# Kernel tuning notes

Hardware: AMD Instinct MI355X
Metric: run time of the kernel (lower is better)

The kernel has to match this reference:

```python
import jax, jax.numpy as jnp
import numpy as np

STRIDE, PAD, DIL, KH, KW = 1, 1, 1, 3, 3


def _bilinear_gather(img, y, xq):
    # img: (Cin,H,W); y,xq: (K,Ho,Wo) float sample coords. Zero padding outside.
    H, W = img.shape[1], img.shape[2]
    y0 = jnp.floor(y); x0 = jnp.floor(xq)
    wy1 = y - y0; wx1 = xq - x0
    wy0 = 1.0 - wy1; wx0 = 1.0 - wx1

    def g(yi, xi):
        valid = (yi >= 0) & (yi <= H - 1) & (xi >= 0) & (xi <= W - 1)
        yc = jnp.clip(yi, 0, H - 1).astype(jnp.int32)
        xc = jnp.clip(xi, 0, W - 1).astype(jnp.int32)
        v = img[:, yc, xc]  # (Cin,K,Ho,Wo)
        return jnp.where(valid[None], v, 0.0)

    return ((wy0 * wx0)[None] * g(y0, x0) + (wy0 * wx1)[None] * g(y0, x0 + 1)
            + (wy1 * wx0)[None] * g(y0 + 1, x0) + (wy1 * wx1)[None] * g(y0 + 1, x0 + 1))


def _deform_conv2d(x, offset, weight, bias):
    B, Cin, H, W = x.shape
    Cout = weight.shape[0]
    Ho, Wo = offset.shape[2], offset.shape[3]
    K = KH * KW
    off = offset.reshape(B, K, 2, Ho, Wo)  # (y,x) pairs per kernel tap, row-major
    ki, kj = jnp.meshgrid(jnp.arange(KH), jnp.arange(KW), indexing='ij')
    base_y = (jnp.arange(Ho) * STRIDE - PAD)[None, :, None] + (ki.reshape(K) * DIL)[:, None, None]  # (K,Ho,1)
    base_x = (jnp.arange(Wo) * STRIDE - PAD)[None, None, :] + (kj.reshape(K) * DIL)[:, None, None]  # (K,1,Wo)
    ys = base_y.astype(x.dtype) + off[:, :, 0]  # (B,K,Ho,Wo)
    xs = base_x.astype(x.dtype) + off[:, :, 1]
    samples = jax.vmap(_bilinear_gather)(x, ys, xs)  # (B,Cin,K,Ho,Wo)
    out = jnp.einsum('bckhw,ock->bohw', samples, weight.reshape(Cout, Cin, K))
    return out + bias[None, :, None, None]


def setup_inputs() -> dict:
    key = jax.random.key(0)
    k1, k2, k3, k4, k5 = jax.random.split(key, 5)
    x = jax.random.normal(k1, (8, 64, 96, 96), dtype=jnp.float32)
    offset = jax.random.normal(k2, (8, 18, 96, 96), dtype=jnp.float32)
    x2 = jax.random.normal(k3, (8, 64, 96, 96), dtype=jnp.float32)
    weight = jax.random.normal(k4, (64, 64, 3, 3), dtype=jnp.float32) * 0.04  # ~kaiming scale for fan_in=576
    bias = jax.random.normal(k5, (64,), dtype=jnp.float32) * 0.1
    return {'x': x, 'offset': offset, 'x2': x2, 'weight': weight, 'bias': bias}


def reference(x, offset, x2, weight, bias):
    out = _deform_conv2d(x, offset, weight, bias)
    out = out + x2
    return jnp.clip(out, 0.0, 6.0)  # ReLU6
```

## Files before the change

### kernel.cpp

```cpp
#include <hip/hip_runtime.h>
#include <math.h>

#define B_    8
#define CIN   64
#define COUT  64
#define H_    96
#define W_    96
#define HW    9216
#define KK    9
#define PIX   64
#define NTHR  256
#define BLKS_PER_B 144
#define SP    72

typedef __attribute__((ext_vector_type(8))) short short8;
typedef __attribute__((ext_vector_type(4))) float floatx4;

static __device__ __forceinline__ unsigned short f2bf(float f) {
    unsigned u = __float_as_uint(f);
    unsigned r = (u + 0x7FFFu + ((u >> 16) & 1u)) >> 16;
    return (unsigned short)r;
}
static __device__ __forceinline__ float bf_lo(unsigned u) { return __uint_as_float(u << 16); }
static __device__ __forceinline__ float bf_hi(unsigned u) { return __uint_as_float(u & 0xFFFF0000u); }

__global__ __launch_bounds__(256) void prep_w_kernel(const float* __restrict__ w,
                                                     unsigned short* __restrict__ wA) {
    int gid  = blockIdx.x * 256 + threadIdx.x;
    int lane = gid & 63;
    int wq   = (gid >> 6) & 3;
    int kap  = gid >> 8;
    int o    = wq * 16 + (lane & 15);
    int cb   = (kap & 1) * 32 + (lane >> 4) * 8;
    int tap  = kap >> 1;
    short8 v;
    #pragma unroll
    for (int j = 0; j < 8; ++j)
        v[j] = (short)f2bf(w[o * 576 + (cb + j) * 9 + tap]);
    *(short8*)&wA[(size_t)gid * 8] = v;
}

__global__ __launch_bounds__(256) void nhwc_bf16_kernel(const float* __restrict__ x,
                                                        unsigned int* __restrict__ xTu) {
    __shared__ float tile[64][65];
    int b   = blockIdx.x / BLKS_PER_B;
    int hw0 = (blockIdx.x % BLKS_PER_B) * 64;
    int lane = threadIdx.x & 63;
    int r    = threadIdx.x >> 6;
    const float* xb = x + (size_t)b * CIN * HW;
    #pragma unroll
    for (int i = 0; i < 16; ++i) {
        int c = r + i * 4;
        tile[c][lane] = xb[(size_t)c * HW + hw0 + lane];
    }
    __syncthreads();
    unsigned int* dst = xTu + ((size_t)b * HW + hw0) * 32;
    int c2 = threadIdx.x & 31;
    int pr = threadIdx.x >> 5;
    #pragma unroll
    for (int i = 0; i < 8; ++i) {
        int p = pr + i * 8;
        unsigned pk = (unsigned)f2bf(tile[2 * c2][p]) |
                      ((unsigned)f2bf(tile[2 * c2 + 1][p]) << 16);
        dst[(size_t)p * 32 + c2] = pk;
    }
}

__global__ __launch_bounds__(256, 4) void deform_mfma_kernel(
    const unsigned int* __restrict__ xTu, const float* __restrict__ offset,
    const float* __restrict__ x2, const float* __restrict__ bias,
    const unsigned short* __restrict__ wA, float* __restrict__ out)
{
    __shared__ float4 ew4[KK * PIX];
    __shared__ int4   eo4[KK * PIX];
    __shared__ __align__(16) short S[2][PIX * SP];

    const int tid  = threadIdx.x;
    const int b    = blockIdx.x & 7;
    const int pix0 = (blockIdx.x >> 3) * PIX;
    const int lane = tid & 63;
    const int wq   = __builtin_amdgcn_readfirstlane(tid >> 6);

    const unsigned int* xb = xTu + (size_t)b * HW * 32;
    const float* offb = offset + (size_t)b * (18 * HW);

    const short8* wAv = (const short8*)wA;
    const int abase = wq * 64 + lane;

    short8 a0 = wAv[abase];
    short8 a1 = wAv[abase + 4 * 64];

    for (int e = tid; e < KK * PIX; e += NTHR) {
        int k  = e >> 6;
        int p  = e & 63;
        int hw = pix0 + p;
        int h  = hw / W_;
        int w  = hw - h * W_;
        float offy = offb[(size_t)(2 * k) * HW + hw];
        float offx = offb[(size_t)(2 * k + 1) * HW + hw];
        int ki = k / 3;
        int kj = k - ki * 3;
        float yy = (float)(h - 1 + ki) + offy;
        float xx = (float)(w - 1 + kj) + offx;
        float y0f = floorf(yy), x0f = floorf(xx);
        float wy1 = yy - y0f, wx1 = xx - x0f;
        float wy0 = 1.0f - wy1, wx0 = 1.0f - wx1;
        int y0 = (int)y0f, x0 = (int)x0f;
        int y1 = y0 + 1, x1 = x0 + 1;
        float vy0 = (y0 >= 0 && y0 < H_) ? 1.0f : 0.0f;
        float vy1 = (y1 >= 0 && y1 < H_) ? 1.0f : 0.0f;
        float vx0 = (x0 >= 0 && x0 < W_) ? 1.0f : 0.0f;
        float vx1 = (x1 >= 0 && x1 < W_) ? 1.0f : 0.0f;
        int y0c = min(max(y0, 0), H_ - 1), y1c = min(max(y1, 0), H_ - 1);
        int x0c = min(max(x0, 0), W_ - 1), x1c = min(max(x1, 0), W_ - 1);
        ew4[e] = make_float4(wy0 * wx0 * vy0 * vx0,
                             wy0 * wx1 * vy0 * vx1,
                             wy1 * wx0 * vy1 * vx0,
                             wy1 * wx1 * vy1 * vx1);
        eo4[e] = make_int4(y0c * W_ + x0c, y0c * W_ + x1c,
                           y1c * W_ + x0c, y1c * W_ + x1c);
    }

    floatx4 acc[4];
    #pragma unroll
    for (int nt = 0; nt < 4; ++nt) acc[nt] = (floatx4){0.f, 0.f, 0.f, 0.f};

    __syncthreads();

    const int c2   = lane & 31;
    const int half = lane >> 5;

    for (int t = 0; t < KK; ++t) {
        const int buf = t & 1;

        short8 n0, n1;
        if (t < KK - 1) {
            n0 = wAv[abase + (8 * (t + 1)) * 64];
            n1 = wAv[abase + (8 * (t + 1) + 4) * 64];
        }

        {
            unsigned int* Su = (unsigned int*)&S[buf][0];
            #pragma unroll
            for (int j = 0; j < 8; ++j) {
                int p = wq * 16 + j * 2 + half;
                int e = t * 64 + p;
                float4 w4 = ew4[e];
                int4   o4 = eo4[e];
                unsigned u0 = xb[((size_t)o4.x << 5) + c2];
                unsigned u1 = xb[((size_t)o4.y << 5) + c2];
                unsigned u2 = xb[((size_t)o4.z << 5) + c2];
                unsigned u3 = xb[((size_t)o4.w << 5) + c2];
                float vl = w4.x * bf_lo(u0);
                vl = fmaf(w4.y, bf_lo(u1), vl);
                vl = fmaf(w4.z, bf_lo(u2), vl);
                vl = fmaf(w4.w, bf_lo(u3), vl);
                float vh = w4.x * bf_hi(u0);
                vh = fmaf(w4.y, bf_hi(u1), vh);
                vh = fmaf(w4.z, bf_hi(u2), vh);
                vh = fmaf(w4.w, bf_hi(u3), vh);
                Su[p * (SP / 2) + c2] = (unsigned)f2bf(vl) | ((unsigned)f2bf(vh) << 16);
            }
        }
        __syncthreads();

        {
            const int n = lane & 15;
            const int qk = (lane >> 4) * 8;
            #pragma unroll
            for (int nt = 0; nt < 4; ++nt) {
                int p = nt * 16 + n;
                short8 b0 = *(const short8*)&S[buf][p * SP + qk];
                short8 b1 = *(const short8*)&S[buf][p * SP + 32 + qk];
                acc[nt] = __builtin_amdgcn_mfma_f32_16x16x32_bf16(a0, b0, acc[nt], 0, 0, 0);
                acc[nt] = __builtin_amdgcn_mfma_f32_16x16x32_bf16(a1, b1, acc[nt], 0, 0, 0);
            }
        }

        a0 = n0;
        a1 = n1;
    }

    {
        const int n = lane & 15;
        const int orow = wq * 16 + (lane >> 4) * 4;
        float bia[4];
        #pragma unroll
        for (int reg = 0; reg < 4; ++reg) bia[reg] = bias[orow + reg];
        #pragma unroll
        for (int nt = 0; nt < 4; ++nt) {
            int hw = pix0 + nt * 16 + n;
            #pragma unroll
            for (int reg = 0; reg < 4; ++reg) {
                size_t idx = ((size_t)(b * COUT + orow + reg)) * HW + hw;
                float r = acc[nt][reg] + bia[reg] + x2[idx];
                r = fminf(fmaxf(r, 0.0f), 6.0f);
                out[idx] = r;
            }
        }
    }
}

__global__ __launch_bounds__(256, 4) void deform_nchw_kernel(
    const float* __restrict__ x, const float* __restrict__ offset,
    const float* __restrict__ x2, const float* __restrict__ weight,
    const float* __restrict__ bias, float* __restrict__ out)
{
    __shared__ float sT[CIN * PIX];
    __shared__ float ewS[4][KK * PIX];
    __shared__ int   eoS[4][KK * PIX];

    const int tid  = threadIdx.x;
    const int b    = blockIdx.x / BLKS_PER_B;
    const int pix0 = (blockIdx.x % BLKS_PER_B) * PIX;
    const int lane = tid & 63;
    const int wq   = __builtin_amdgcn_readfirstlane(tid >> 6);

    const float* xb   = x + (size_t)b * (CIN * HW);
    const float* offb = offset + (size_t)b * (18 * HW);

    for (int e = tid; e < KK * PIX; e += NTHR) {
        int k  = e >> 6;
        int p  = e & 63;
        int hw = pix0 + p;
        int h  = hw / W_;
        int w  = hw - h * W_;
        float offy = offb[(size_t)(2 * k) * HW + hw];
        float offx = offb[(size_t)(2 * k + 1) * HW + hw];
        int ki = k / 3;
        int kj = k - ki * 3;
        float yy = (float)(h - 1 + ki) + offy;
        float xx = (float)(w - 1 + kj) + offx;
        float y0f = floorf(yy), x0f = floorf(xx);
        float wy1 = yy - y0f, wx1 = xx - x0f;
        float wy0 = 1.0f - wy1, wx0 = 1.0f - wx1;
        int y0 = (int)y0f, x0 = (int)x0f;
        int y1 = y0 + 1, x1 = x0 + 1;
        float vy0 = (y0 >= 0 && y0 < H_) ? 1.0f : 0.0f;
        float vy1 = (y1 >= 0 && y1 < H_) ? 1.0f : 0.0f;
        float vx0 = (x0 >= 0 && x0 < W_) ? 1.0f : 0.0f;
        float vx1 = (x1 >= 0 && x1 < W_) ? 1.0f : 0.0f;
        int y0c = min(max(y0, 0), H_ - 1), y1c = min(max(y1, 0), H_ - 1);
        int x0c = min(max(x0, 0), W_ - 1), x1c = min(max(x1, 0), W_ - 1);
        ewS[0][e] = wy0 * wx0 * vy0 * vx0;
        ewS[1][e] = wy0 * wx1 * vy0 * vx1;
        ewS[2][e] = wy1 * wx0 * vy1 * vx0;
        ewS[3][e] = wy1 * wx1 * vy1 * vx1;
        eoS[0][e] = y0c * W_ + x0c;
        eoS[1][e] = y0c * W_ + x1c;
        eoS[2][e] = y1c * W_ + x0c;
        eoS[3][e] = y1c * W_ + x1c;
    }

    float acc[16];
    #pragma unroll
    for (int i = 0; i < 16; ++i) acc[i] = 0.0f;

    __syncthreads();

    for (int k = 0; k < KK; ++k) {
        {
            const int eb = k * 64 + lane;
            const float w0 = ewS[0][eb], w1 = ewS[1][eb], w2 = ewS[2][eb], w3 = ewS[3][eb];
            const int   o0 = eoS[0][eb], o1 = eoS[1][eb], o2 = eoS[2][eb], o3 = eoS[3][eb];
            const int cg = tid >> 6;
            const float* xc = xb + (size_t)(cg * 16) * HW;
            #pragma unroll
            for (int i = 0; i < 16; ++i) {
                float v = w0 * xc[o0] + w1 * xc[o1] + w2 * xc[o2] + w3 * xc[o3];
                sT[(cg * 16 + i) * 64 + lane] = v;
                xc += HW;
            }
        }
        __syncthreads();
        {
            #pragma unroll 2
            for (int c = 0; c < 64; ++c) {
                float sv = sT[c * 64 + lane];
                #pragma unroll
                for (int oi = 0; oi < 16; ++oi)
                    acc[oi] = fmaf(weight[(wq * 16 + oi) * 576 + c * 9 + k], sv, acc[oi]);
            }
        }
        __syncthreads();
    }

    const size_t obase = ((size_t)b * COUT + wq * 16) * HW + pix0 + lane;
    #pragma unroll
    for (int oi = 0; oi < 16; ++oi) {
        float r = acc[oi] + bias[wq * 16 + oi] + x2[obase + (size_t)oi * HW];
        r = fminf(fmaxf(r, 0.0f), 6.0f);
        out[obase + (size_t)oi * HW] = r;
    }
}

extern "C" void kernel_launch(void* const* d_in, const int* in_sizes, int n_in,
                              void* d_out, int out_size, void* d_ws, size_t ws_size,
                              hipStream_t stream) {
    const float* x      = (const float*)d_in[0];
    const float* offset = (const float*)d_in[1];
    const float* x2     = (const float*)d_in[2];
    const float* weight = (const float*)d_in[3];
    const float* bias   = (const float*)d_in[4];
    float* out          = (float*)d_out;

    const int grid = B_ * BLKS_PER_B;

    const size_t xT_bytes = (size_t)B_ * HW * CIN * sizeof(unsigned short);
    const size_t wA_bytes = (size_t)18 * 4 * 64 * 8 * sizeof(unsigned short);

    if (ws_size >= xT_bytes + wA_bytes) {
        unsigned int*   xTu = (unsigned int*)d_ws;
        unsigned short* wA  = (unsigned short*)((char*)d_ws + xT_bytes);
        prep_w_kernel<<<18, 256, 0, stream>>>(weight, wA);
        nhwc_bf16_kernel<<<grid, 256, 0, stream>>>(x, xTu);
        deform_mfma_kernel<<<grid, NTHR, 0, stream>>>(xTu, offset, x2, bias, wA, out);
    } else {
        deform_nchw_kernel<<<grid, NTHR, 0, stream>>>(x, offset, x2, weight, bias, out);
    }
}
```

Before: 135.0 us.

## Prefetch next tap's gathers during MFMA, compress sample tables, merge prep kernels

The main loop now issues the global gathers for tap t+1 into registers before running the MFMAs for tap t, so gather latency can overlap matrix work. The per-sample bilinear tables shrink to bf16 separable row/column weights plus ushort offsets, which cuts LDS footprint and traffic. The weight and NHWC prep kernels are merged into one launch. The prefetch holds 32 extra registers per thread under launch_bounds(256,4), which may cause spills or lower occupancy, and bf16 weights add small rounding error.

```diff
diff --git a/kernel.cpp b/kernel.cpp
--- a/kernel.cpp
+++ b/kernel.cpp
@@ -24,45 +24,85 @@
 static __device__ __forceinline__ float bf_lo(unsigned u) { return __uint_as_float(u << 16); }
 static __device__ __forceinline__ float bf_hi(unsigned u) { return __uint_as_float(u & 0xFFFF0000u); }
 
-__global__ __launch_bounds__(256) void prep_w_kernel(const float* __restrict__ w,
-                                                     unsigned short* __restrict__ wA) {
-    int gid  = blockIdx.x * 256 + threadIdx.x;
-    int lane = gid & 63;
-    int wq   = (gid >> 6) & 3;
-    int kap  = gid >> 8;
-    int o    = wq * 16 + (lane & 15);
-    int cb   = (kap & 1) * 32 + (lane >> 4) * 8;
-    int tap  = kap >> 1;
-    short8 v;
-    #pragma unroll
-    for (int j = 0; j < 8; ++j)
-        v[j] = (short)f2bf(w[o * 576 + (cb + j) * 9 + tap]);
-    *(short8*)&wA[(size_t)gid * 8] = v;
-}
-
-__global__ __launch_bounds__(256) void nhwc_bf16_kernel(const float* __restrict__ x,
-                                                        unsigned int* __restrict__ xTu) {
+__global__ __launch_bounds__(256) void prep_kernel(const float* __restrict__ x,
+                                                   const float* __restrict__ w,
+                                                   unsigned int* __restrict__ xTu,
+                                                   unsigned short* __restrict__ wA) {
     __shared__ float tile[64][65];
-    int b   = blockIdx.x / BLKS_PER_B;
-    int hw0 = (blockIdx.x % BLKS_PER_B) * 64;
-    int lane = threadIdx.x & 63;
-    int r    = threadIdx.x >> 6;
-    const float* xb = x + (size_t)b * CIN * HW;
-    #pragma unroll
-    for (int i = 0; i < 16; ++i) {
-        int c = r + i * 4;
-        tile[c][lane] = xb[(size_t)c * HW + hw0 + lane];
-    }
-    __syncthreads();
-    unsigned int* dst = xTu + ((size_t)b * HW + hw0) * 32;
-    int c2 = threadIdx.x & 31;
-    int pr = threadIdx.x >> 5;
-    #pragma unroll
-    for (int i = 0; i < 8; ++i) {
-        int p = pr + i * 8;
-        unsigned pk = (unsigned)f2bf(tile[2 * c2][p]) |
-                      ((unsigned)f2bf(tile[2 * c2 + 1][p]) << 16);
-        dst[(size_t)p * 32 + c2] = pk;
+    if (blockIdx.x < B_ * BLKS_PER_B) {
+        int b   = blockIdx.x / BLKS_PER_B;
+        int hw0 = (blockIdx.x % BLKS_PER_B) * 64;
+        int lane = threadIdx.x & 63;
+        int r    = threadIdx.x >> 6;
+        const float* xb = x + (size_t)b * CIN * HW;
+        #pragma unroll
+        for (int i = 0; i < 16; ++i) {
+            int c = r + i * 4;
+            tile[c][lane] = xb[(size_t)c * HW + hw0 + lane];
+        }
+        __syncthreads();
+        unsigned int* dst = xTu + ((size_t)b * HW + hw0) * 32;
+        int c2 = threadIdx.x & 31;
+        int pr = threadIdx.x >> 5;
+        #pragma unroll
+        for (int i = 0; i < 8; ++i) {
+            int p = pr + i * 8;
+            unsigned pk = (unsigned)f2bf(tile[2 * c2][p]) |
+                          ((unsigned)f2bf(tile[2 * c2 + 1][p]) << 16);
+            dst[(size_t)p * 32 + c2] = pk;
+        }
+    } else {
+        int gid  = (blockIdx.x - B_ * BLKS_PER_B) * 256 + threadIdx.x;
+        int lane = gid & 63;
+        int wq   = (gid >> 6) & 3;
+        int kap  = gid >> 8;
+        int o    = wq * 16 + (lane & 15);
+        int cb   = (kap & 1) * 32 + (lane >> 4) * 8;
+        int tap  = kap >> 1;
+        short8 v;
+        #pragma unroll
+        for (int j = 0; j < 8; ++j)
+            v[j] = (short)f2bf(w[o * 576 + (cb + j) * 9 + tap]);
+        *(short8*)&wA[(size_t)gid * 8] = v;
+    }
+}
+
+static __device__ __forceinline__ void issue_tap_loads(
+    const unsigned int* __restrict__ xb, const ushort4* eoS,
+    int t, int wq, int half, int c2, unsigned u[8][4])
+{
+    #pragma unroll
+    for (int j = 0; j < 8; ++j) {
+        int p = wq * 16 + j * 2 + half;
+        ushort4 o4 = eoS[t * 64 + p];
+        u[j][0] = xb[((size_t)o4.x << 5) + c2];
+        u[j][1] = xb[((size_t)o4.y << 5) + c2];
+        u[j][2] = xb[((size_t)o4.z << 5) + c2];
+        u[j][3] = xb[((size_t)o4.w << 5) + c2];
+    }
+}
+
+static __device__ __forceinline__ void compute_tap(
+    const uint2* awS, short* Sbuf, int t, int wq, int half, int c2,
+    const unsigned u[8][4])
+{
+    unsigned int* Su = (unsigned int*)Sbuf;
+    #pragma unroll
+    for (int j = 0; j < 8; ++j) {
+        int p = wq * 16 + j * 2 + half;
+        uint2 aw = awS[t * 64 + p];
+        float ay0 = bf_lo(aw.x), ay1 = bf_hi(aw.x);
+        float ax0 = bf_lo(aw.y), ax1 = bf_hi(aw.y);
+        float w00 = ay0 * ax0, w01 = ay0 * ax1, w10 = ay1 * ax0, w11 = ay1 * ax1;
+        float vl = w00 * bf_lo(u[j][0]);
+        vl = fmaf(w01, bf_lo(u[j][1]), vl);
+        vl = fmaf(w10, bf_lo(u[j][2]), vl);
+        vl = fmaf(w11, bf_lo(u[j][3]), vl);
+        float vh = w00 * bf_hi(u[j][0]);
+        vh = fmaf(w01, bf_hi(u[j][1]), vh);
+        vh = fmaf(w10, bf_hi(u[j][2]), vh);
+        vh = fmaf(w11, bf_hi(u[j][3]), vh);
+        Su[p * (SP / 2) + c2] = (unsigned)f2bf(vl) | ((unsigned)f2bf(vh) << 16);
     }
 }
 
@@ -71,8 +111,8 @@
     const float* __restrict__ x2, const float* __restrict__ bias,
     const unsigned short* __restrict__ wA, float* __restrict__ out)
 {
-    __shared__ float4 ew4[KK * PIX];
-    __shared__ int4   eo4[KK * PIX];
+    __shared__ uint2   awS[KK * PIX];
+    __shared__ ushort4 eoS[KK * PIX];
     __shared__ __align__(16) short S[2][PIX * SP];
 
     const int tid  = threadIdx.x;
@@ -107,18 +147,18 @@
         float wy0 = 1.0f - wy1, wx0 = 1.0f - wx1;
         int y0 = (int)y0f, x0 = (int)x0f;
         int y1 = y0 + 1, x1 = x0 + 1;
-        float vy0 = (y0 >= 0 && y0 < H_) ? 1.0f : 0.0f;
-        float vy1 = (y1 >= 0 && y1 < H_) ? 1.0f : 0.0f;
-        float vx0 = (x0 >= 0 && x0 < W_) ? 1.0f : 0.0f;
-        float vx1 = (x1 >= 0 && x1 < W_) ? 1.0f : 0.0f;
+        float ay0 = (y0 >= 0 && y0 < H_) ? wy0 : 0.0f;
+        float ay1 = (y1 >= 0 && y1 < H_) ? wy1 : 0.0f;
+        float ax0 = (x0 >= 0 && x0 < W_) ? wx0 : 0.0f;
+        float ax1 = (x1 >= 0 && x1 < W_) ? wx1 : 0.0f;
         int y0c = min(max(y0, 0), H_ - 1), y1c = min(max(y1, 0), H_ - 1);
         int x0c = min(max(x0, 0), W_ - 1), x1c = min(max(x1, 0), W_ - 1);
-        ew4[e] = make_float4(wy0 * wx0 * vy0 * vx0,
-                             wy0 * wx1 * vy0 * vx1,
-                             wy1 * wx0 * vy1 * vx0,
-                             wy1 * wx1 * vy1 * vx1);
-        eo4[e] = make_int4(y0c * W_ + x0c, y0c * W_ + x1c,
-                           y1c * W_ + x0c, y1c * W_ + x1c);
+        awS[e] = make_uint2((unsigned)f2bf(ay0) | ((unsigned)f2bf(ay1) << 16),
+                            (unsigned)f2bf(ax0) | ((unsigned)f2bf(ax1) << 16));
+        eoS[e] = make_ushort4((unsigned short)(y0c * W_ + x0c),
+                              (unsigned short)(y0c * W_ + x1c),
+                              (unsigned short)(y1c * W_ + x0c),
+                              (unsigned short)(y1c * W_ + x1c));
     }
 
     floatx4 acc[4];
@@ -130,39 +170,21 @@
     const int c2   = lane & 31;
     const int half = lane >> 5;
 
+    unsigned u[8][4];
+    issue_tap_loads(xb, eoS, 0, wq, half, c2, u);
+
     for (int t = 0; t < KK; ++t) {
         const int buf = t & 1;
 
+        compute_tap(awS, &S[buf][0], t, wq, half, c2, u);
+        __syncthreads();
+
         short8 n0, n1;
         if (t < KK - 1) {
+            issue_tap_loads(xb, eoS, t + 1, wq, half, c2, u);
             n0 = wAv[abase + (8 * (t + 1)) * 64];
             n1 = wAv[abase + (8 * (t + 1) + 4) * 64];
         }
-
-        {
-            unsigned int* Su = (unsigned int*)&S[buf][0];
-            #pragma unroll
-            for (int j = 0; j < 8; ++j) {
-                int p = wq * 16 + j * 2 + half;
-                int e = t * 64 + p;
-                float4 w4 = ew4[e];
-                int4   o4 = eo4[e];
-                unsigned u0 = xb[((size_t)o4.x << 5) + c2];
-                unsigned u1 = xb[((size_t)o4.y << 5) + c2];
-                unsigned u2 = xb[((size_t)o4.z << 5) + c2];
-                unsigned u3 = xb[((size_t)o4.w << 5) + c2];
-                float vl = w4.x * bf_lo(u0);
-                vl = fmaf(w4.y, bf_lo(u1), vl);
-                vl = fmaf(w4.z, bf_lo(u2), vl);
-                vl = fmaf(w4.w, bf_lo(u3), vl);
-                float vh = w4.x * bf_hi(u0);
-                vh = fmaf(w4.y, bf_hi(u1), vh);
-                vh = fmaf(w4.z, bf_hi(u2), vh);
-                vh = fmaf(w4.w, bf_hi(u3), vh);
-                Su[p * (SP / 2) + c2] = (unsigned)f2bf(vl) | ((unsigned)f2bf(vh) << 16);
-            }
-        }
-        __syncthreads();
 
         {
             const int n = lane & 15;
@@ -312,8 +334,7 @@
     if (ws_size >= xT_bytes + wA_bytes) {
         unsigned int*   xTu = (unsigned int*)d_ws;
         unsigned short* wA  = (unsigned short*)((char*)d_ws + xT_bytes);
-        prep_w_kernel<<<18, 256, 0, stream>>>(weight, wA);
-        nhwc_bf16_kernel<<<grid, 256, 0, stream>>>(x, xTu);
+        prep_kernel<<<grid + 18, 256, 0, stream>>>(x, weight, xTu, wA);
         deform_mfma_kernel<<<grid, NTHR, 0, stream>>>(xTu, offset, x2, bias, wA, out);
     } else {
         deform_nchw_kernel<<<grid, NTHR, 0, stream>>>(x, offset, x2, weight, bias, out);
```

New measurement: 124.0 us. -8.2%, faster.
